# Optimization experiments

Measured on AMD Instinct MI355X. Metric: run time of the kernel, lower is better.

Reference implementation:

```python
import jax, jax.numpy as jnp
import numpy as np

THRESHOLD = 0.5
CONNECT_EPS = 0.1


def setup_inputs() -> dict:
    key = jax.random.key(0)
    ks = jax.random.split(key, 8)
    B, N, F = 4, 512, 128
    H = jax.random.normal(ks[0], (B, N, F), dtype=jnp.float32)
    A = jax.random.uniform(ks[1], (B, N, N), dtype=jnp.float32)
    s2f, sf = 1.0 / np.sqrt(2 * F), 1.0 / np.sqrt(F)
    dW1 = jax.random.normal(ks[2], (2 * F, F), dtype=jnp.float32) * s2f
    db1 = jnp.zeros((F,), dtype=jnp.float32)
    dW2 = jax.random.normal(ks[3], (F, 1), dtype=jnp.float32) * sf
    db2 = jnp.zeros((1,), dtype=jnp.float32)
    rW1 = jax.random.normal(ks[4], (2 * F + 1, F), dtype=jnp.float32) * s2f
    rb1 = jnp.zeros((F,), dtype=jnp.float32)
    rW2 = jax.random.normal(ks[5], (F, F), dtype=jnp.float32) * sf
    rb2 = jnp.zeros((F,), dtype=jnp.float32)
    return {"H": H, "A": A, "dW1": dW1, "db1": db1, "dW2": dW2, "db2": db2,
            "rW1": rW1, "rb1": rb1, "rW2": rW2, "rb2": rb2}


def reference(H, A, dW1, db1, dW2, db2, rW1, rb1, rW2, rb2):
    B, N, F = H.shape
    # Detector on pairs [H_i ; H_j]: split the first linear so we never build [B,N,N,2F].
    Hi = jnp.einsum('bnf,fh->bnh', H, dW1[:F])           # [B,N,F]
    Hj = jnp.einsum('bnf,fh->bnh', H, dW1[F:])           # [B,N,F]
    h = jax.nn.elu(Hi[:, :, None, :] + Hj[:, None, :, :] + db1)  # [B,N,N,F]
    scores = jax.nn.sigmoid(jnp.einsum('bijh,ho->bijo', h, dW2)[..., 0] + db2[0])  # [B,N,N]
    connected = A > CONNECT_EPS
    contradictions = jnp.where(connected, scores, 0.0)
    max_contra = contradictions.max(axis=-1)             # [B,N]
    contra_mask = max_contra > THRESHOLD                 # [B,N] bool
    # Neighbor mean over A > 0 (strict zero, matching torch.where(A[b,n] > 0))
    nbr = (A > 0).astype(H.dtype)                        # [B,N,N]
    deg = nbr.sum(axis=-1)                               # [B,N]
    neighbor_feat = jnp.einsum('bij,bjf->bif', nbr, H) / jnp.maximum(deg, 1.0)[..., None]
    concat = jnp.concatenate([H, neighbor_feat, max_contra[..., None]], axis=-1)  # [B,N,2F+1]
    res = jax.nn.elu(jnp.einsum('bnf,fh->bnh', concat, rW1) + rb1)
    res = jnp.einsum('bnh,ho->bno', res, rW2) + rb2       # [B,N,F]
    update = contra_mask & (deg > 0)
    H_resolved = jnp.where(update[..., None], res, H)
    return H_resolved, contra_mask
```

## Files before the change

kernel.cpp:

```cpp
#include <hip/hip_runtime.h>
#include <cmath>

#define B_ 4
#define N_ 512
#define F_ 128
#define BN_ (B_*N_)
#define NG_ (BN_/4)

__device__ __forceinline__ float elu_f(float x) {
    return fmaxf(x, __expf(fminf(x, 0.f)) - 1.f);
}

__global__ __launch_bounds__(512, 4) void k_pre(
    const float* __restrict__ H, const float* __restrict__ dW1,
    const float* __restrict__ db1,
    float* __restrict__ Hi, float* __restrict__ EHi, float* __restrict__ HjT,
    float* __restrict__ csp) {
    __shared__ float sH[4][F_];
    __shared__ float sPA[3][4][F_], sPB[3][4][F_];
    const int t = threadIdx.x;
    const int f = t & 127;
    const int kq = t >> 7;
    if (blockIdx.x < NG_) {
        const int row0 = blockIdx.x * 4;
        const int b  = row0 >> 9;
        const int n0 = row0 & 511;
        sH[kq][f] = H[(size_t)(row0 + kq) * F_ + f];
        __syncthreads();
        float accA[4] = {0.f,0.f,0.f,0.f}, accB[4] = {0.f,0.f,0.f,0.f};
        const int k0 = kq * 32;
        #pragma unroll 4
        for (int k = k0; k < k0 + 32; ++k) {
            const float wa = dW1[(size_t)k * F_ + f];
            const float wb = dW1[(size_t)(F_ + k) * F_ + f];
            #pragma unroll
            for (int r = 0; r < 4; ++r) {
                accA[r] = fmaf(sH[r][k], wa, accA[r]);
                accB[r] = fmaf(sH[r][k], wb, accB[r]);
            }
        }
        if (kq > 0) {
            #pragma unroll
            for (int r = 0; r < 4; ++r) {
                sPA[kq - 1][r][f] = accA[r];
                sPB[kq - 1][r][f] = accB[r];
            }
        }
        __syncthreads();
        if (kq == 0) {
            const float bias = db1[f];
            float bsum[4];
            #pragma unroll
            for (int r = 0; r < 4; ++r) {
                const float av = accA[r] + sPA[0][r][f] + sPA[1][r][f]
                               + sPA[2][r][f] + bias;
                Hi [(size_t)(row0 + r) * F_ + f] = av;
                EHi[(size_t)(row0 + r) * F_ + f] = __expf(av);
                bsum[r] = accB[r] + sPB[0][r][f] + sPB[1][r][f] + sPB[2][r][f];
            }
            float4 hv;
            hv.x = bsum[0]; hv.y = bsum[1]; hv.z = bsum[2]; hv.w = bsum[3];
            *reinterpret_cast<float4*>(HjT + ((size_t)b * F_ + f) * N_ + n0) = hv;
        }
    } else {
        const int bx = blockIdx.x - NG_;
        const int b  = bx >> 3;
        const int e  = bx & 7;
        float s = 0.f;
        const float* hp = H + ((size_t)b * N_ + e * 64 + kq * 16) * F_ + f;
        #pragma unroll 4
        for (int jj = 0; jj < 16; ++jj) s += hp[(size_t)jj * F_];
        sH[kq][f] = s;
        __syncthreads();
        if (kq == 0)
            csp[((size_t)b * 8 + e) * F_ + f] =
                sH[0][f] + sH[1][f] + sH[2][f] + sH[3][f];
    }
}

#define SCORE_F(HJ4, CP) {                                                    \
    const float ejx = __expf((HJ4).x), ejy = __expf((HJ4).y),                 \
                ejz = __expf((HJ4).z), ejw = __expf((HJ4).w);                 \
    const float wv_ = wq.CP;                                                  \
    acc0.x = fmaf(__builtin_amdgcn_fmed3f(h0.CP + (HJ4).x, fmaf(e0.CP, ejx, -1.f), 0.f), wv_, acc0.x); \
    acc0.y = fmaf(__builtin_amdgcn_fmed3f(h0.CP + (HJ4).y, fmaf(e0.CP, ejy, -1.f), 0.f), wv_, acc0.y); \
    acc0.z = fmaf(__builtin_amdgcn_fmed3f(h0.CP + (HJ4).z, fmaf(e0.CP, ejz, -1.f), 0.f), wv_, acc0.z); \
    acc0.w = fmaf(__builtin_amdgcn_fmed3f(h0.CP + (HJ4).w, fmaf(e0.CP, ejw, -1.f), 0.f), wv_, acc0.w); \
    acc1.x = fmaf(__builtin_amdgcn_fmed3f(h1.CP + (HJ4).x, fmaf(e1.CP, ejx, -1.f), 0.f), wv_, acc1.x); \
    acc1.y = fmaf(__builtin_amdgcn_fmed3f(h1.CP + (HJ4).y, fmaf(e1.CP, ejy, -1.f), 0.f), wv_, acc1.y); \
    acc1.z = fmaf(__builtin_amdgcn_fmed3f(h1.CP + (HJ4).z, fmaf(e1.CP, ejz, -1.f), 0.f), wv_, acc1.z); \
    acc1.w = fmaf(__builtin_amdgcn_fmed3f(h1.CP + (HJ4).w, fmaf(e1.CP, ejw, -1.f), 0.f), wv_, acc1.w); \
    acc2.x = fmaf(__builtin_amdgcn_fmed3f(h2.CP + (HJ4).x, fmaf(e2.CP, ejx, -1.f), 0.f), wv_, acc2.x); \
    acc2.y = fmaf(__builtin_amdgcn_fmed3f(h2.CP + (HJ4).y, fmaf(e2.CP, ejy, -1.f), 0.f), wv_, acc2.y); \
    acc2.z = fmaf(__builtin_amdgcn_fmed3f(h2.CP + (HJ4).z, fmaf(e2.CP, ejz, -1.f), 0.f), wv_, acc2.z); \
    acc2.w = fmaf(__builtin_amdgcn_fmed3f(h2.CP + (HJ4).w, fmaf(e2.CP, ejw, -1.f), 0.f), wv_, acc2.w); \
    acc3.x = fmaf(__builtin_amdgcn_fmed3f(h3.CP + (HJ4).x, fmaf(e3.CP, ejx, -1.f), 0.f), wv_, acc3.x); \
    acc3.y = fmaf(__builtin_amdgcn_fmed3f(h3.CP + (HJ4).y, fmaf(e3.CP, ejy, -1.f), 0.f), wv_, acc3.y); \
    acc3.z = fmaf(__builtin_amdgcn_fmed3f(h3.CP + (HJ4).z, fmaf(e3.CP, ejz, -1.f), 0.f), wv_, acc3.z); \
    acc3.w = fmaf(__builtin_amdgcn_fmed3f(h3.CP + (HJ4).w, fmaf(e3.CP, ejw, -1.f), 0.f), wv_, acc3.w); }

#define LOADQ(QQ, B0, B1, B2, B3)                                             \
    B0 = *reinterpret_cast<const float4*>(hjq + (size_t)((QQ) * 4 + 0) * N_); \
    B1 = *reinterpret_cast<const float4*>(hjq + (size_t)((QQ) * 4 + 1) * N_); \
    B2 = *reinterpret_cast<const float4*>(hjq + (size_t)((QQ) * 4 + 2) * N_); \
    B3 = *reinterpret_cast<const float4*>(hjq + (size_t)((QQ) * 4 + 3) * N_);

#define COMPQ(QQ, B0, B1, B2, B3) {                                           \
    const int q_ = kq * 8 + (QQ);                                             \
    const float4 h0 = sU[q_][0], h1 = sU[q_][1], h2 = sU[q_][2], h3 = sU[q_][3]; \
    const float4 e0 = sU[q_][4], e1 = sU[q_][5], e2 = sU[q_][6], e3 = sU[q_][7]; \
    const float4 wq = sU[q_][8];                                              \
    SCORE_F(B0, x) SCORE_F(B1, y) SCORE_F(B2, z) SCORE_F(B3, w) }

__global__ __launch_bounds__(512) void k_score(
    const float* __restrict__ Hi, const float* __restrict__ EHi,
    const float* __restrict__ HjT, const float* __restrict__ A,
    const float* __restrict__ dW2, const float* __restrict__ db2,
    float* __restrict__ maxcv, float* __restrict__ degv,
    unsigned long long* __restrict__ zmask, float* __restrict__ maskout) {
    __shared__ float4 sU[32][9];
    __shared__ float  sAcc[4][4][N_];
    __shared__ float  red_mx[8][4];
    __shared__ int    red_cnt[8][4];
    const int t = threadIdx.x;
    const int lane = t & 63;
    const int w = t >> 6;
    const int u  = t & 127;
    const int kq = t >> 7;
    const int bi0 = blockIdx.x * 4;
    const int b = bi0 >> 9;

    if (t < 288) {
        const int q  = t / 9;
        const int sl = t - q * 9;
        const float* src = (sl < 4) ? (Hi  + (size_t)(bi0 + sl)     * F_ + 4 * q)
                         : (sl < 8) ? (EHi + (size_t)(bi0 + sl - 4) * F_ + 4 * q)
                                    : (dW2 + 4 * q);
        sU[q][sl] = *reinterpret_cast<const float4*>(src);
    }
    float a_r[4];
    #pragma unroll
    for (int r = 0; r < 4; ++r) a_r[r] = A[(size_t)(bi0 + r) * N_ + t];

    const float* __restrict__ hjq = HjT + (size_t)b * F_ * N_
                                  + (size_t)(kq * 32) * N_ + 4 * u;
    float4 hA0, hA1, hA2, hA3, hB0, hB1, hB2, hB3;
    LOADQ(0, hA0, hA1, hA2, hA3)
    __syncthreads();

    float4 acc0 = {0.f,0.f,0.f,0.f}, acc1 = {0.f,0.f,0.f,0.f};
    float4 acc2 = {0.f,0.f,0.f,0.f}, acc3 = {0.f,0.f,0.f,0.f};

    LOADQ(1, hB0, hB1, hB2, hB3)
    COMPQ(0, hA0, hA1, hA2, hA3)
    LOADQ(2, hA0, hA1, hA2, hA3)
    COMPQ(1, hB0, hB1, hB2, hB3)
    LOADQ(3, hB0, hB1, hB2, hB3)
    COMPQ(2, hA0, hA1, hA2, hA3)
    LOADQ(4, hA0, hA1, hA2, hA3)
    COMPQ(3, hB0, hB1, hB2, hB3)
    LOADQ(5, hB0, hB1, hB2, hB3)
    COMPQ(4, hA0, hA1, hA2, hA3)
    LOADQ(6, hA0, hA1, hA2, hA3)
    COMPQ(5, hB0, hB1, hB2, hB3)
    LOADQ(7, hB0, hB1, hB2, hB3)
    COMPQ(6, hA0, hA1, hA2, hA3)
    COMPQ(7, hB0, hB1, hB2, hB3)

    *reinterpret_cast<float4*>(&sAcc[kq][0][4 * u]) = acc0;
    *reinterpret_cast<float4*>(&sAcc[kq][1][4 * u]) = acc1;
    *reinterpret_cast<float4*>(&sAcc[kq][2][4 * u]) = acc2;
    *reinterpret_cast<float4*>(&sAcc[kq][3][4 * u]) = acc3;
    __syncthreads();

    #pragma unroll
    for (int r = 0; r < 4; ++r) {
        const float a = a_r[r];
        const float sum = sAcc[0][r][t] + sAcc[1][r][t]
                        + sAcc[2][r][t] + sAcc[3][r][t];
        float mx = (a > 0.1f) ? sum : -INFINITY;
        #pragma unroll
        for (int off = 1; off < 64; off <<= 1)
            mx = fmaxf(mx, __shfl_xor(mx, off));
        const unsigned long long pos = __ballot(a > 0.f);
        const unsigned long long zb  = __ballot(a <= 0.f);
        if (lane == 0) {
            red_mx[w][r]  = mx;
            red_cnt[w][r] = (int)__popcll(pos);
            zmask[(size_t)(bi0 + r) * 8 + w] = zb;
        }
    }
    __syncthreads();
    if (t < 4) {
        float m = -INFINITY; int c = 0;
        #pragma unroll
        for (int ww = 0; ww < 8; ++ww) {
            m = fmaxf(m, red_mx[ww][t]);
            c += red_cnt[ww][t];
        }
        const float mc = (m > -INFINITY)
                       ? 1.f / (1.f + __expf(-(m + db2[0]))) : 0.f;
        maxcv[bi0 + t] = mc;
        degv[bi0 + t]  = (float)c;
        maskout[bi0 + t] = (mc > 0.5f) ? 1.f : 0.f;
    }
}

__global__ __launch_bounds__(512, 4) void k_mlp(
    const float* __restrict__ H, const float* __restrict__ csp,
    const unsigned long long* __restrict__ zmask,
    const float* __restrict__ degv, const float* __restrict__ maxcv,
    const float* __restrict__ rW1, const float* __restrict__ rb1,
    const float* __restrict__ rW2, const float* __restrict__ rb2,
    float* __restrict__ out) {
    __shared__ float sC[4][260];
    __shared__ float sP[3][4][F_];
    __shared__ float sL1[4][F_];
    __shared__ float sMC[4], sDegF[4];
    const int t  = threadIdx.x;
    const int f  = t & 127;
    const int kq = t >> 7;
    const int row0 = blockIdx.x * 4;
    const int b = row0 >> 9;

    {
        const int row = row0 + kq;
        sC[kq][f] = H[(size_t)row * F_ + f];
        float cs = 0.f;
        #pragma unroll
        for (int e = 0; e < 8; ++e)
            cs += csp[((size_t)b * 8 + e) * F_ + f];
        #pragma unroll
        for (int wv = 0; wv < 8; ++wv) {
            unsigned long long zb = zmask[(size_t)row * 8 + wv];
            while (zb) {
                const int j = __ffsll(zb) - 1;
                zb &= zb - 1;
                cs -= H[((size_t)b * N_ + wv * 64 + j) * F_ + f];
            }
        }
        sC[kq][F_ + f] = cs / fmaxf(degv[row], 1.f);
    }
    if (t < 4) {
        sMC[t]   = maxcv[row0 + t];
        sDegF[t] = degv[row0 + t];
    }
    __syncthreads();

    float macc[4];
    {
        const float bias = rb1[f];
        #pragma unroll
        for (int r = 0; r < 4; ++r) macc[r] = (kq == 0) ? bias : 0.f;
    }
    const int k0 = kq * 64;
    #pragma unroll 4
    for (int k = k0; k < k0 + 64; ++k) {
        const float wv = rW1[(size_t)k * F_ + f];
        #pragma unroll
        for (int r = 0; r < 4; ++r) macc[r] = fmaf(sC[r][k], wv, macc[r]);
    }
    if (kq == 3) {
        const float w256 = rW1[(size_t)256 * F_ + f];
        #pragma unroll
        for (int r = 0; r < 4; ++r) macc[r] = fmaf(sMC[r], w256, macc[r]);
    }
    if (kq > 0) {
        #pragma unroll
        for (int r = 0; r < 4; ++r) sP[kq - 1][r][f] = macc[r];
    }
    __syncthreads();
    if (kq == 0) {
        #pragma unroll
        for (int r = 0; r < 4; ++r)
            sL1[r][f] = elu_f(macc[r] + sP[0][r][f] + sP[1][r][f] + sP[2][r][f]);
    }
    __syncthreads();

    float macc2[4];
    {
        const float bias2 = rb2[f];
        #pragma unroll
        for (int r = 0; r < 4; ++r) macc2[r] = (kq == 0) ? bias2 : 0.f;
    }
    const int m0k = kq * 32;
    #pragma unroll 4
    for (int k = m0k; k < m0k + 32; ++k) {
        const float wv = rW2[(size_t)k * F_ + f];
        #pragma unroll
        for (int r = 0; r < 4; ++r) macc2[r] = fmaf(sL1[r][k], wv, macc2[r]);
    }
    if (kq > 0) {
        #pragma unroll
        for (int r = 0; r < 4; ++r) sP[kq - 1][r][f] = macc2[r];
    }
    __syncthreads();
    if (kq == 0) {
        #pragma unroll
        for (int r = 0; r < 4; ++r) {
            const int row = row0 + r;
            const float res = macc2[r] + sP[0][r][f] + sP[1][r][f] + sP[2][r][f];
            const bool upd = (sMC[r] > 0.5f) && (sDegF[r] > 0.f);
            out[(size_t)row * F_ + f] = upd ? res : sC[r][f];
        }
    }
}

extern "C" void kernel_launch(void* const* d_in, const int* in_sizes, int n_in,
                              void* d_out, int out_size, void* d_ws, size_t ws_size,
                              hipStream_t stream) {
    const float* H   = (const float*)d_in[0];
    const float* A   = (const float*)d_in[1];
    const float* dW1 = (const float*)d_in[2];
    const float* db1 = (const float*)d_in[3];
    const float* dW2 = (const float*)d_in[4];
    const float* db2 = (const float*)d_in[5];
    const float* rW1 = (const float*)d_in[6];
    const float* rb1 = (const float*)d_in[7];
    const float* rW2 = (const float*)d_in[8];
    const float* rb2 = (const float*)d_in[9];

    float* ws   = (float*)d_ws;
    float* Hi   = ws;
    float* EHi  = Hi   + BN_ * F_;
    float* HjT  = EHi  + BN_ * F_;
    float* csp  = HjT  + BN_ * F_;
    float* degv = csp  + B_ * 8 * F_;
    float* maxc = degv + BN_;
    unsigned long long* zmask =
        (unsigned long long*)(maxc + BN_);

    float* out      = (float*)d_out;
    float* mask_out = out + BN_ * F_;

    k_pre  <<<NG_ + 32, 512, 0, stream>>>(H, dW1, db1, Hi, EHi, HjT, csp);
    k_score<<<NG_, 512, 0, stream>>>(Hi, EHi, HjT, A, dW2, db2,
                                     maxc, degv, zmask, mask_out);
    k_mlp  <<<NG_, 512, 0, stream>>>(H, csp, zmask, degv, maxc,
                                     rW1, rb1, rW2, rb2, out);
}
```

Baseline: 40.87 us.

## Fuse score kernel and resolver MLP kernel into one launch

Merges k_score and k_mlp into a single kernel k_main that runs the residual MLP right after the contradiction reduction. Per-row max contradiction, degree and zero-adjacency bitmasks stay in shared memory instead of a global round trip. The score accumulation buffer is reused for the MLP scratch arrays. This removes one kernel launch and its global writes and reads, but the fused kernel needs more registers and shared memory, which can lower occupancy for the MLP phase.

```diff
diff --git a/kernel.cpp b/kernel.cpp
--- a/kernel.cpp
+++ b/kernel.cpp
@@ -112,21 +112,26 @@
     const float4 wq = sU[q_][8];                                              \
     SCORE_F(B0, x) SCORE_F(B1, y) SCORE_F(B2, z) SCORE_F(B3, w) }
 
-__global__ __launch_bounds__(512) void k_score(
+__global__ __launch_bounds__(512) void k_main(
     const float* __restrict__ Hi, const float* __restrict__ EHi,
     const float* __restrict__ HjT, const float* __restrict__ A,
     const float* __restrict__ dW2, const float* __restrict__ db2,
-    float* __restrict__ maxcv, float* __restrict__ degv,
-    unsigned long long* __restrict__ zmask, float* __restrict__ maskout) {
+    const float* __restrict__ H, const float* __restrict__ csp,
+    const float* __restrict__ rW1, const float* __restrict__ rb1,
+    const float* __restrict__ rW2, const float* __restrict__ rb2,
+    float* __restrict__ out, float* __restrict__ maskout) {
     __shared__ float4 sU[32][9];
-    __shared__ float  sAcc[4][4][N_];
+    __shared__ float  sBig[4 * 4 * N_];
     __shared__ float  red_mx[8][4];
     __shared__ int    red_cnt[8][4];
+    __shared__ unsigned long long sZb[8][4];
+    __shared__ float  sMC[4], sDegF[4];
     const int t = threadIdx.x;
     const int lane = t & 63;
     const int w = t >> 6;
     const int u  = t & 127;
     const int kq = t >> 7;
+    const int f  = t & 127;
     const int bi0 = blockIdx.x * 4;
     const int b = bi0 >> 9;
 
@@ -167,17 +172,17 @@
     COMPQ(6, hA0, hA1, hA2, hA3)
     COMPQ(7, hB0, hB1, hB2, hB3)
 
-    *reinterpret_cast<float4*>(&sAcc[kq][0][4 * u]) = acc0;
-    *reinterpret_cast<float4*>(&sAcc[kq][1][4 * u]) = acc1;
-    *reinterpret_cast<float4*>(&sAcc[kq][2][4 * u]) = acc2;
-    *reinterpret_cast<float4*>(&sAcc[kq][3][4 * u]) = acc3;
+    *reinterpret_cast<float4*>(&sBig[(kq * 4 + 0) * N_ + 4 * u]) = acc0;
+    *reinterpret_cast<float4*>(&sBig[(kq * 4 + 1) * N_ + 4 * u]) = acc1;
+    *reinterpret_cast<float4*>(&sBig[(kq * 4 + 2) * N_ + 4 * u]) = acc2;
+    *reinterpret_cast<float4*>(&sBig[(kq * 4 + 3) * N_ + 4 * u]) = acc3;
     __syncthreads();
 
     #pragma unroll
     for (int r = 0; r < 4; ++r) {
         const float a = a_r[r];
-        const float sum = sAcc[0][r][t] + sAcc[1][r][t]
-                        + sAcc[2][r][t] + sAcc[3][r][t];
+        const float sum = sBig[(0 * 4 + r) * N_ + t] + sBig[(1 * 4 + r) * N_ + t]
+                        + sBig[(2 * 4 + r) * N_ + t] + sBig[(3 * 4 + r) * N_ + t];
         float mx = (a > 0.1f) ? sum : -INFINITY;
         #pragma unroll
         for (int off = 1; off < 64; off <<= 1)
@@ -187,7 +192,7 @@
         if (lane == 0) {
             red_mx[w][r]  = mx;
             red_cnt[w][r] = (int)__popcll(pos);
-            zmask[(size_t)(bi0 + r) * 8 + w] = zb;
+            sZb[w][r]     = zb;
         }
     }
     __syncthreads();
@@ -200,50 +205,33 @@
         }
         const float mc = (m > -INFINITY)
                        ? 1.f / (1.f + __expf(-(m + db2[0]))) : 0.f;
-        maxcv[bi0 + t] = mc;
-        degv[bi0 + t]  = (float)c;
+        sMC[t]   = mc;
+        sDegF[t] = (float)c;
         maskout[bi0 + t] = (mc > 0.5f) ? 1.f : 0.f;
     }
-}
-
-__global__ __launch_bounds__(512, 4) void k_mlp(
-    const float* __restrict__ H, const float* __restrict__ csp,
-    const unsigned long long* __restrict__ zmask,
-    const float* __restrict__ degv, const float* __restrict__ maxcv,
-    const float* __restrict__ rW1, const float* __restrict__ rb1,
-    const float* __restrict__ rW2, const float* __restrict__ rb2,
-    float* __restrict__ out) {
-    __shared__ float sC[4][260];
-    __shared__ float sP[3][4][F_];
-    __shared__ float sL1[4][F_];
-    __shared__ float sMC[4], sDegF[4];
-    const int t  = threadIdx.x;
-    const int f  = t & 127;
-    const int kq = t >> 7;
-    const int row0 = blockIdx.x * 4;
-    const int b = row0 >> 9;
+    __syncthreads();
+
+    float* sC  = sBig;
+    float* sP  = sBig + 1040;
+    float* sL1 = sBig + 2576;
 
     {
-        const int row = row0 + kq;
-        sC[kq][f] = H[(size_t)row * F_ + f];
+        const int row = bi0 + kq;
+        sC[kq * 260 + f] = H[(size_t)row * F_ + f];
         float cs = 0.f;
         #pragma unroll
         for (int e = 0; e < 8; ++e)
             cs += csp[((size_t)b * 8 + e) * F_ + f];
         #pragma unroll
         for (int wv = 0; wv < 8; ++wv) {
-            unsigned long long zb = zmask[(size_t)row * 8 + wv];
+            unsigned long long zb = sZb[wv][kq];
             while (zb) {
                 const int j = __ffsll(zb) - 1;
                 zb &= zb - 1;
                 cs -= H[((size_t)b * N_ + wv * 64 + j) * F_ + f];
             }
         }
-        sC[kq][F_ + f] = cs / fmaxf(degv[row], 1.f);
-    }
-    if (t < 4) {
-        sMC[t]   = maxcv[row0 + t];
-        sDegF[t] = degv[row0 + t];
+        sC[kq * 260 + F_ + f] = cs / fmaxf(sDegF[kq], 1.f);
     }
     __syncthreads();
 
@@ -258,7 +246,7 @@
     for (int k = k0; k < k0 + 64; ++k) {
         const float wv = rW1[(size_t)k * F_ + f];
         #pragma unroll
-        for (int r = 0; r < 4; ++r) macc[r] = fmaf(sC[r][k], wv, macc[r]);
+        for (int r = 0; r < 4; ++r) macc[r] = fmaf(sC[r * 260 + k], wv, macc[r]);
     }
     if (kq == 3) {
         const float w256 = rW1[(size_t)256 * F_ + f];
@@ -267,13 +255,15 @@
     }
     if (kq > 0) {
         #pragma unroll
-        for (int r = 0; r < 4; ++r) sP[kq - 1][r][f] = macc[r];
+        for (int r = 0; r < 4; ++r) sP[((kq - 1) * 4 + r) * F_ + f] = macc[r];
     }
     __syncthreads();
     if (kq == 0) {
         #pragma unroll
         for (int r = 0; r < 4; ++r)
-            sL1[r][f] = elu_f(macc[r] + sP[0][r][f] + sP[1][r][f] + sP[2][r][f]);
+            sL1[r * F_ + f] = elu_f(macc[r] + sP[(0 * 4 + r) * F_ + f]
+                                   + sP[(1 * 4 + r) * F_ + f]
+                                   + sP[(2 * 4 + r) * F_ + f]);
     }
     __syncthreads();
 
@@ -288,20 +278,22 @@
     for (int k = m0k; k < m0k + 32; ++k) {
         const float wv = rW2[(size_t)k * F_ + f];
         #pragma unroll
-        for (int r = 0; r < 4; ++r) macc2[r] = fmaf(sL1[r][k], wv, macc2[r]);
+        for (int r = 0; r < 4; ++r) macc2[r] = fmaf(sL1[r * F_ + k], wv, macc2[r]);
     }
     if (kq > 0) {
         #pragma unroll
-        for (int r = 0; r < 4; ++r) sP[kq - 1][r][f] = macc2[r];
+        for (int r = 0; r < 4; ++r) sP[((kq - 1) * 4 + r) * F_ + f] = macc2[r];
     }
     __syncthreads();
     if (kq == 0) {
         #pragma unroll
         for (int r = 0; r < 4; ++r) {
-            const int row = row0 + r;
-            const float res = macc2[r] + sP[0][r][f] + sP[1][r][f] + sP[2][r][f];
+            const int row = bi0 + r;
+            const float res = macc2[r] + sP[(0 * 4 + r) * F_ + f]
+                            + sP[(1 * 4 + r) * F_ + f]
+                            + sP[(2 * 4 + r) * F_ + f];
             const bool upd = (sMC[r] > 0.5f) && (sDegF[r] > 0.f);
-            out[(size_t)row * F_ + f] = upd ? res : sC[r][f];
+            out[(size_t)row * F_ + f] = upd ? res : sC[r * 260 + f];
         }
     }
 }
@@ -320,22 +312,17 @@
     const float* rW2 = (const float*)d_in[8];
     const float* rb2 = (const float*)d_in[9];
 
-    float* ws   = (float*)d_ws;
-    float* Hi   = ws;
-    float* EHi  = Hi   + BN_ * F_;
-    float* HjT  = EHi  + BN_ * F_;
-    float* csp  = HjT  + BN_ * F_;
-    float* degv = csp  + B_ * 8 * F_;
-    float* maxc = degv + BN_;
-    unsigned long long* zmask =
-        (unsigned long long*)(maxc + BN_);
+    float* ws  = (float*)d_ws;
+    float* Hi  = ws;
+    float* EHi = Hi  + BN_ * F_;
+    float* HjT = EHi + BN_ * F_;
+    float* csp = HjT + BN_ * F_;
 
     float* out      = (float*)d_out;
     float* mask_out = out + BN_ * F_;
 
-    k_pre  <<<NG_ + 32, 512, 0, stream>>>(H, dW1, db1, Hi, EHi, HjT, csp);
-    k_score<<<NG_, 512, 0, stream>>>(Hi, EHi, HjT, A, dW2, db2,
-                                     maxc, degv, zmask, mask_out);
-    k_mlp  <<<NG_, 512, 0, stream>>>(H, csp, zmask, degv, maxc,
-                                     rW1, rb1, rW2, rb2, out);
+    k_pre <<<NG_ + 32, 512, 0, stream>>>(H, dW1, db1, Hi, EHi, HjT, csp);
+    k_main<<<NG_, 512, 0, stream>>>(Hi, EHi, HjT, A, dW2, db2,
+                                    H, csp, rW1, rb1, rW2, rb2,
+                                    out, mask_out);
 }
```

Result: slower. 41.93 us (+2.6%).
